# Performance work log

Hardware: AMD Instinct MI355X
Metric: run time of the kernel (lower is better)

The kernel has to match this reference:

```python
import jax, jax.numpy as jnp
import numpy as np

N = 1_000_000   # total elements
G = 100_000     # number of groups (all guaranteed non-empty)
D = 128         # emb_dim


def setup_inputs() -> dict:
    key = jax.random.key(0)
    k1, k2, k3, k4, k5, k6 = jax.random.split(key, 6)
    embeddings = jax.random.normal(k1, (N, D), dtype=jnp.float32)
    # sorted segment ids with every id in [0, G) present at least once
    extra = jax.random.randint(k2, (N - G,), 0, G, dtype=jnp.int32)
    seg_ids = jnp.sort(jnp.concatenate([jnp.arange(G, dtype=jnp.int32), extra]))
    # nn.Linear default init: U(-1/sqrt(fan_in), 1/sqrt(fan_in))
    s = 1.0 / np.sqrt(D)
    Wq = jax.random.uniform(k3, (D, D), jnp.float32, -s, s)
    bq = jax.random.uniform(k4, (D,), jnp.float32, -s, s)
    Wk = jax.random.uniform(k5, (D, D), jnp.float32, -s, s)
    bk = jax.random.uniform(k6, (D,), jnp.float32, -s, s)
    return {"embeddings": embeddings, "seg_ids": seg_ids,
            "Wq": Wq, "bq": bq, "Wk": Wk, "bk": bk}


def reference(embeddings, seg_ids, Wq, bq, Wk, bk):
    # keys = key_layer(embeddings), computed once for all elements  [N, D]
    keys = embeddings @ Wk.T + bk
    # index of the LAST element of each (sorted, contiguous) segment
    counts = jax.ops.segment_sum(jnp.ones_like(seg_ids), seg_ids, num_segments=G)
    last_idx = jnp.cumsum(counts) - 1                       # [G]
    # query = query_layer(group_emb[-1])                    [G, D]
    q = embeddings[last_idx] @ Wq.T + bq
    # per-element attention logit: <q[group(i)], keys[i]>   [N]
    logits = jnp.sum(q[seg_ids] * keys, axis=-1)
    # segment-wise stable softmax
    m = jax.ops.segment_max(logits, seg_ids, num_segments=G)
    e = jnp.exp(logits - m[seg_ids])
    denom = jax.ops.segment_sum(e, seg_ids, num_segments=G)
    w = e / denom[seg_ids]                                  # [N]
    # weighted sum of keys per segment                      [G, D]
    out = jax.ops.segment_sum(w[:, None] * keys, seg_ids, num_segments=G)
    return out
```

## Files before the change

kernel.cpp:

```cpp
#include <hip/hip_runtime.h>
#include <math.h>

typedef _Float16 half8  __attribute__((ext_vector_type(8)));
typedef _Float16 half2v __attribute__((ext_vector_type(2)));
typedef float    floatx4 __attribute__((ext_vector_type(4)));

#define LGKM_FENCE() asm volatile("s_waitcnt lgkmcnt(0)" ::: "memory")

__global__ void seg_bounds_kernel(const int* __restrict__ seg,
                                  int* __restrict__ seg_start, int N, int G) {
    int i = blockIdx.x * 256 + threadIdx.x;
    if (i >= N) return;
    int s = seg[i];
    if (i == 0 || s != seg[i - 1]) seg_start[s] = i;
    if (i == N - 1) seg_start[G] = N;
}

__device__ inline half8 pack8(float4 a, float4 b) {
    half8 r;
    r[0] = (_Float16)a.x; r[1] = (_Float16)a.y; r[2] = (_Float16)a.z; r[3] = (_Float16)a.w;
    r[4] = (_Float16)b.x; r[5] = (_Float16)b.y; r[6] = (_Float16)b.z; r[7] = (_Float16)b.w;
    return r;
}

__global__ __launch_bounds__(64, 1) void fused_attn_kernel(
    const float* __restrict__ emb, const int* __restrict__ seg_start,
    const float* __restrict__ Wq, const float* __restrict__ bq,
    const float* __restrict__ Wk, const float* __restrict__ bk,
    float* __restrict__ out)
{
    __shared__ alignas(16) _Float16 keys_lds[16][136];
    __shared__ alignas(16) _Float16 q_lds[8][136];
    __shared__ alignas(16) float    L_lds[16];

    const int lane = threadIdx.x;
    const int m    = lane & 15;
    const int quad = lane >> 4;

    const int g0 = blockIdx.x * 8;
    const int lo = seg_start[g0 + (m & 7)];
    const int hi = seg_start[g0 + (m & 7) + 1];
    const int s0 = __shfl(lo, 0);
    const int e0 = __shfl(hi, 7);

    float bkv[8];
#pragma unroll
    for (int c = 0; c < 8; ++c) bkv[c] = bk[16 * c + m];

    {
        long qrow = (long)hi - 1;
        half8 aq[4];
#pragma unroll
        for (int kq = 0; kq < 4; ++kq) {
            const float4* p = (const float4*)(emb + qrow * 128 + kq * 32 + quad * 8);
            aq[kq] = pack8(p[0], p[1]);
        }
#pragma unroll
        for (int c = 0; c < 8; ++c) {
            float bqc = bq[16 * c + m];
            floatx4 acc = {bqc, bqc, bqc, bqc};
#pragma unroll
            for (int kq = 0; kq < 4; ++kq) {
                const float4* wp = (const float4*)(Wq + (16 * c + m) * 128 + kq * 32 + quad * 8);
                half8 bf = pack8(wp[0], wp[1]);
                acc = __builtin_amdgcn_mfma_f32_16x16x32_f16(aq[kq], bf, acc, 0, 0, 0);
            }
            if (quad < 2) {
#pragma unroll
                for (int r = 0; r < 4; ++r)
                    q_lds[quad * 4 + r][16 * c + m] = (_Float16)acc[r];
            }
        }
    }
    LGKM_FENCE();

    half8 qf[4];
#pragma unroll
    for (int kq = 0; kq < 4; ++kq)
        qf[kq] = *(const half8*)&q_lds[m & 7][kq * 32 + quad * 8];

    half8 wkf[8][4];
#pragma unroll
    for (int c = 0; c < 8; ++c)
#pragma unroll
        for (int kq = 0; kq < 4; ++kq) {
            const float4* wp = (const float4*)(Wk + (16 * c + m) * 128 + kq * 32 + quad * 8);
            wkf[c][kq] = pack8(wp[0], wp[1]);
        }

    const int nt = (e0 - s0 + 15) >> 4;

    float4 pre[8];
    {
        long prow = (long)min(s0 + m, e0 - 1);
#pragma unroll
        for (int kq = 0; kq < 4; ++kq) {
            const float4* p = (const float4*)(emb + prow * 128 + kq * 32 + quad * 8);
            pre[2 * kq] = p[0]; pre[2 * kq + 1] = p[1];
        }
    }

    int   g = g0;
    int   cur_end = __shfl(hi, 0);
    float M_run = -INFINITY;
    float M_cur = 0.f;
    float d_acc = 0.f, acc0 = 0.f, acc1 = 0.f;

    for (int tt = 0; tt < nt; ++tt) {
        const int t   = s0 + tt * 16;
        const int cnt = min(16, e0 - t);

        half8 ak[4];
#pragma unroll
        for (int kq = 0; kq < 4; ++kq)
            ak[kq] = pack8(pre[2 * kq], pre[2 * kq + 1]);

        if (tt + 1 < nt) {
            long nrow = (long)min(t + 16 + m, e0 - 1);
#pragma unroll
            for (int kq = 0; kq < 4; ++kq) {
                const float4* p = (const float4*)(emb + nrow * 128 + kq * 32 + quad * 8);
                pre[2 * kq] = p[0]; pre[2 * kq + 1] = p[1];
            }
        }

#pragma unroll
        for (int c = 0; c < 8; ++c) {
            floatx4 acc = {bkv[c], bkv[c], bkv[c], bkv[c]};
#pragma unroll
            for (int kq = 0; kq < 4; ++kq)
                acc = __builtin_amdgcn_mfma_f32_16x16x32_f16(ak[kq], wkf[c][kq], acc, 0, 0, 0);
#pragma unroll
            for (int r = 0; r < 4; ++r)
                keys_lds[quad * 4 + r][16 * c + m] = (_Float16)acc[r];
        }
        LGKM_FENCE();

        floatx4 lacc = {0.f, 0.f, 0.f, 0.f};
#pragma unroll
        for (int kq = 0; kq < 4; ++kq) {
            half8 af = *(const half8*)&keys_lds[m][kq * 32 + quad * 8];
            lacc = __builtin_amdgcn_mfma_f32_16x16x32_f16(af, qf[kq], lacc, 0, 0, 0);
        }
#pragma unroll
        for (int r = 0; r < 4; ++r) {
            int rowc = t + quad * 4 + r;
            if (m < 8 && rowc >= lo && rowc < hi) L_lds[quad * 4 + r] = lacc[r];
        }
        LGKM_FENCE();

        float lg[16];
#pragma unroll
        for (int i = 0; i < 4; ++i) {
            float4 v = *(const float4*)&L_lds[4 * i];
            lg[4 * i] = v.x; lg[4 * i + 1] = v.y; lg[4 * i + 2] = v.z; lg[4 * i + 3] = v.w;
        }
        half2v kv[16];
#pragma unroll
        for (int r = 0; r < 16; ++r)
            kv[r] = *(const half2v*)&keys_lds[r][2 * lane];

        float tm = -INFINITY;
#pragma unroll
        for (int r = 0; r < 16; ++r) {
            int row = t + r;
            tm = fmaxf(tm, (row >= lo && row < hi) ? lg[r] : -INFINITY);
        }
        float M_new = fmaxf(M_run, tm);
        float sc = (M_run == -INFINITY) ? 0.f : __expf(M_run - M_new);
        M_run = M_new;

        float sc_c = __shfl(sc, g - g0);
        M_cur      = __shfl(M_new, g - g0);
        acc0 *= sc_c; acc1 *= sc_c; d_acc *= sc_c;

#pragma unroll
        for (int rl = 0; rl < 16; ++rl) {
            if (rl < cnt) {
                int row = t + rl;
                while (row >= cur_end) {
                    float inv = 1.0f / d_acc;
                    float2 o; o.x = acc0 * inv; o.y = acc1 * inv;
                    *(float2*)(out + (long)g * 128 + 2 * lane) = o;
                    ++g;
                    cur_end = __shfl(hi, g - g0);
                    M_cur   = __shfl(M_new, g - g0);
                    acc0 = 0.f; acc1 = 0.f; d_acc = 0.f;
                }
                float e = __expf(lg[rl] - M_cur);
                acc0  += e * (float)kv[rl][0];
                acc1  += e * (float)kv[rl][1];
                d_acc += e;
            }
        }
    }
    {
        float inv = 1.0f / d_acc;
        float2 o; o.x = acc0 * inv; o.y = acc1 * inv;
        *(float2*)(out + (long)g * 128 + 2 * lane) = o;
    }
}

extern "C" void kernel_launch(void* const* d_in, const int* in_sizes, int n_in,
                              void* d_out, int out_size, void* d_ws, size_t ws_size,
                              hipStream_t stream) {
    const float* emb = (const float*)d_in[0];
    const int*   seg = (const int*)d_in[1];
    const float* Wq  = (const float*)d_in[2];
    const float* bq  = (const float*)d_in[3];
    const float* Wk  = (const float*)d_in[4];
    const float* bk  = (const float*)d_in[5];
    float* out = (float*)d_out;

    const int N = in_sizes[1];
    const int G = out_size / 128;

    int* seg_start = (int*)d_ws;

    seg_bounds_kernel<<<(N + 255) / 256, 256, 0, stream>>>(seg, seg_start, N, G);
    fused_attn_kernel<<<G / 8, 64, 0, stream>>>(emb, seg_start, Wq, bq, Wk, bk, out);
}
```

Measured before the change: 860.6 us.

## Share Wk fragments in LDS across four waves per block to cut registers

Moves the f16-packed Wk B-fragments out of per-lane registers into shared LDS loaded cooperatively by four waves. Blocks now hold 256 threads, each wave handling 8 groups, and launch bounds target 3 blocks per CU. Dropping the 32 half8 register arrays is meant to raise occupancy and hide global load latency. The cost is LDS reads for every MFMA B operand in the inner loop, plus a block barrier.

After: 752.8 us. 12.5% less time.

```diff
diff --git a/kernel.cpp b/kernel.cpp
--- a/kernel.cpp
+++ b/kernel.cpp
@@ -23,21 +23,36 @@
     return r;
 }
 
-__global__ __launch_bounds__(64, 1) void fused_attn_kernel(
+__global__ __launch_bounds__(256, 3) void fused_attn_kernel(
     const float* __restrict__ emb, const int* __restrict__ seg_start,
     const float* __restrict__ Wq, const float* __restrict__ bq,
     const float* __restrict__ Wk, const float* __restrict__ bk,
     float* __restrict__ out)
 {
-    __shared__ alignas(16) _Float16 keys_lds[16][136];
-    __shared__ alignas(16) _Float16 q_lds[8][136];
-    __shared__ alignas(16) float    L_lds[16];
-
-    const int lane = threadIdx.x;
+    __shared__ alignas(16) half8    wk_lds[8][4][64];
+    __shared__ alignas(16) _Float16 keys_lds[4][16][136];
+    __shared__ alignas(16) float    L_lds[4][16];
+
+    const int tid  = threadIdx.x;
+    const int wave = tid >> 6;
+    const int lane = tid & 63;
     const int m    = lane & 15;
     const int quad = lane >> 4;
 
-    const int g0 = blockIdx.x * 8;
+#pragma unroll
+    for (int i = 0; i < 2; ++i) {
+        int c = 2 * wave + i;
+        const float4* wp0 = (const float4*)(Wk + (16 * c + m) * 128 + 0 * 32 + quad * 8);
+        const float4* wp1 = (const float4*)(Wk + (16 * c + m) * 128 + 1 * 32 + quad * 8);
+        const float4* wp2 = (const float4*)(Wk + (16 * c + m) * 128 + 2 * 32 + quad * 8);
+        const float4* wp3 = (const float4*)(Wk + (16 * c + m) * 128 + 3 * 32 + quad * 8);
+        wk_lds[c][0][lane] = pack8(wp0[0], wp0[1]);
+        wk_lds[c][1][lane] = pack8(wp1[0], wp1[1]);
+        wk_lds[c][2][lane] = pack8(wp2[0], wp2[1]);
+        wk_lds[c][3][lane] = pack8(wp3[0], wp3[1]);
+    }
+
+    const int g0 = (blockIdx.x * 4 + wave) * 8;
     const int lo = seg_start[g0 + (m & 7)];
     const int hi = seg_start[g0 + (m & 7) + 1];
     const int s0 = __shfl(lo, 0);
@@ -68,7 +83,7 @@
             if (quad < 2) {
 #pragma unroll
                 for (int r = 0; r < 4; ++r)
-                    q_lds[quad * 4 + r][16 * c + m] = (_Float16)acc[r];
+                    keys_lds[wave][quad * 4 + r][16 * c + m] = (_Float16)acc[r];
             }
         }
     }
@@ -77,16 +92,9 @@
     half8 qf[4];
 #pragma unroll
     for (int kq = 0; kq < 4; ++kq)
-        qf[kq] = *(const half8*)&q_lds[m & 7][kq * 32 + quad * 8];
-
-    half8 wkf[8][4];
-#pragma unroll
-    for (int c = 0; c < 8; ++c)
-#pragma unroll
-        for (int kq = 0; kq < 4; ++kq) {
-            const float4* wp = (const float4*)(Wk + (16 * c + m) * 128 + kq * 32 + quad * 8);
-            wkf[c][kq] = pack8(wp[0], wp[1]);
-        }
+        qf[kq] = *(const half8*)&keys_lds[wave][m & 7][kq * 32 + quad * 8];
+
+    __syncthreads();
 
     const int nt = (e0 - s0 + 15) >> 4;
 
@@ -128,37 +136,39 @@
         for (int c = 0; c < 8; ++c) {
             floatx4 acc = {bkv[c], bkv[c], bkv[c], bkv[c]};
 #pragma unroll
-            for (int kq = 0; kq < 4; ++kq)
-                acc = __builtin_amdgcn_mfma_f32_16x16x32_f16(ak[kq], wkf[c][kq], acc, 0, 0, 0);
+            for (int kq = 0; kq < 4; ++kq) {
+                half8 bf = wk_lds[c][kq][lane];
+                acc = __builtin_amdgcn_mfma_f32_16x16x32_f16(ak[kq], bf, acc, 0, 0, 0);
+            }
 #pragma unroll
             for (int r = 0; r < 4; ++r)
-                keys_lds[quad * 4 + r][16 * c + m] = (_Float16)acc[r];
+                keys_lds[wave][quad * 4 + r][16 * c + m] = (_Float16)acc[r];
         }
         LGKM_FENCE();
 
         floatx4 lacc = {0.f, 0.f, 0.f, 0.f};
 #pragma unroll
         for (int kq = 0; kq < 4; ++kq) {
-            half8 af = *(const half8*)&keys_lds[m][kq * 32 + quad * 8];
+            half8 af = *(const half8*)&keys_lds[wave][m][kq * 32 + quad * 8];
             lacc = __builtin_amdgcn_mfma_f32_16x16x32_f16(af, qf[kq], lacc, 0, 0, 0);
         }
 #pragma unroll
         for (int r = 0; r < 4; ++r) {
             int rowc = t + quad * 4 + r;
-            if (m < 8 && rowc >= lo && rowc < hi) L_lds[quad * 4 + r] = lacc[r];
+            if (m < 8 && rowc >= lo && rowc < hi) L_lds[wave][quad * 4 + r] = lacc[r];
         }
         LGKM_FENCE();
 
         float lg[16];
 #pragma unroll
         for (int i = 0; i < 4; ++i) {
-            float4 v = *(const float4*)&L_lds[4 * i];
+            float4 v = *(const float4*)&L_lds[wave][4 * i];
             lg[4 * i] = v.x; lg[4 * i + 1] = v.y; lg[4 * i + 2] = v.z; lg[4 * i + 3] = v.w;
         }
         half2v kv[16];
 #pragma unroll
         for (int r = 0; r < 16; ++r)
-            kv[r] = *(const half2v*)&keys_lds[r][2 * lane];
+            kv[r] = *(const half2v*)&keys_lds[wave][r][2 * lane];
 
         float tm = -INFINITY;
 #pragma unroll
@@ -218,5 +228,5 @@
     int* seg_start = (int*)d_ws;
 
     seg_bounds_kernel<<<(N + 255) / 256, 256, 0, stream>>>(seg, seg_start, N, G);
-    fused_attn_kernel<<<G / 8, 64, 0, stream>>>(emb, seg_start, Wq, bq, Wk, bk, out);
-}
+    fused_attn_kernel<<<G / 32, 256, 0, stream>>>(emb, seg_start, Wq, bq, Wk, bk, out);
+}
```
